# Kernel optimization log

Measured on AMD Instinct MI355X. Metric: run time of the kernel, lower is better.

The kernel has to match this reference:

```python
import jax, jax.numpy as jnp
import numpy as np

T, B, I, H, O = 512, 64, 512, 1024, 512
STDV = 1.0 / np.sqrt(H)


def setup_inputs() -> dict:
    key = jax.random.key(0)
    ks = jax.random.split(key, 12)
    u = lambda k, shape: jax.random.uniform(k, shape, jnp.float32, -STDV, STDV)
    return {
        "input": jax.random.normal(ks[0], (T, B, I), jnp.float32),
        "state": jnp.zeros((B, H), jnp.float32),
        "W_zh": u(ks[1], (H, H)), "W_zx": u(ks[2], (I, H)), "b_z": u(ks[3], (H,)),
        "W_rh": u(ks[4], (H, H)), "W_rx": u(ks[5], (I, H)), "b_r": u(ks[6], (H,)),
        "W_hh": u(ks[7], (H, H)), "W_hx": u(ks[8], (I, H)), "b_h": u(ks[9], (H,)),
        "W_out": u(ks[10], (O, H)), "b_out": u(ks[11], (O,)),
    }


def reference(input, state, W_zh, W_zx, b_z, W_rh, W_rx, b_r, W_hh, W_hx, b_h, W_out, b_out):
    # input: [T, B, I]; state: [B, H]
    def step(h, x):
        z = jax.nn.sigmoid(h @ W_zh + x @ W_zx + b_z)
        r = jax.nn.sigmoid(h @ W_rh + x @ W_rx + b_r)
        ht = jnp.tanh((h * r) @ W_hh + x @ W_hx + b_h)
        h = (1.0 - z) * h + z * ht
        y = h @ W_out.T + b_out  # Linear(hidim -> outdim)
        return h, y

    h_final, Y = jax.lax.scan(step, state, input)  # Y: [T, B, O]
    # torch.cat(Y, dim=0) -> [T*B, O]
    return Y.reshape(T * B, O), h_final
```

## Files before the change

### kernel.cpp

```cpp
#include <hip/hip_runtime.h>
#include <cstdint>


#define TT 512
#define BB 64
#define II 512
#define HH 1024
#define OO 512
#define NTHR 1024
#define NBLK 256
#define RSTR 528

typedef float4 f4;
__device__ __forceinline__ f4 ld4(const float* p){ return *reinterpret_cast<const f4*>(p); }
__device__ __forceinline__ int swz(int k){ return k ^ (((k >> 4) & 7) << 2); }

__device__ __forceinline__ void ldc4(const float* p, f4* d){
  asm volatile(
    "global_load_dwordx4 %0, %4, off sc0 sc1\n\t"
    "global_load_dwordx4 %1, %4, off offset:256 sc0 sc1\n\t"
    "global_load_dwordx4 %2, %4, off offset:512 sc0 sc1\n\t"
    "global_load_dwordx4 %3, %4, off offset:768 sc0 sc1\n\t"
    "s_waitcnt vmcnt(0)"
    : "=&v"(d[0]),"=&v"(d[1]),"=&v"(d[2]),"=&v"(d[3])
    : "v"(p) : "memory");
}
__device__ __forceinline__ float ldc1(const float* p){
  float v;
  asm volatile("global_load_dword %0, %1, off sc0 sc1\n\ts_waitcnt vmcnt(0)"
               : "=v"(v) : "v"(p) : "memory");
  return v;
}
__device__ __forceinline__ void stc1(float* p, float v){
  asm volatile("global_store_dword %0, %1, off sc0 sc1" :: "v"(p), "v"(v) : "memory");
}

__global__ void k_transpose_x(const float* __restrict__ x, float* __restrict__ xT){
  size_t total = (size_t)TT * II * BB;
  for (size_t n = (size_t)blockIdx.x * blockDim.x + threadIdx.x; n < total;
       n += (size_t)gridDim.x * blockDim.x){
    size_t t = n / ((size_t)II * BB);
    size_t rem = n % ((size_t)II * BB);
    size_t i = rem / BB, b = rem % BB;
    xT[n] = x[(t * BB + b) * II + i];
  }
}

__global__ void k_transpose_wx(const float* __restrict__ W, float* __restrict__ WT){
  size_t n = (size_t)blockIdx.x * blockDim.x + threadIdx.x;
  if (n >= (size_t)II * HH) return;
  size_t j = n / II, k = n % II;
  WT[n] = W[k * HH + j];
}

__global__ void k_transpose_h0(const float* __restrict__ st, float* __restrict__ h0){
  size_t n = (size_t)blockIdx.x * blockDim.x + threadIdx.x;
  if (n >= (size_t)HH * BB) return;
  size_t j = n / BB, b = n % BB;
  h0[n] = st[b * HH + j];
}

__global__ void k_init_bars(unsigned* bars){
  if (threadIdx.x < 512) bars[threadIdx.x] = 0;
}

__device__ __forceinline__ void g_arrive(unsigned* bars, int bid, unsigned ep){
  asm volatile("s_waitcnt vmcnt(0)" ::: "memory");
  unsigned* leaf = bars + (bid & 15) * 16;
  unsigned old = __hip_atomic_fetch_add(leaf, 1u, __ATOMIC_RELAXED, __HIP_MEMORY_SCOPE_AGENT);
  if (old + 1u == ep * 16u)
    __hip_atomic_fetch_add(bars + 256, 1u, __ATOMIC_RELAXED, __HIP_MEMORY_SCOPE_AGENT);
}
__device__ __forceinline__ void g_wait(unsigned* bars, unsigned ep){
  while (__hip_atomic_load(bars + 256, __ATOMIC_RELAXED, __HIP_MEMORY_SCOPE_AGENT) < ep * 16u)
    __builtin_amdgcn_s_sleep(1);
}

#define WREDUCE(v) { v += __shfl_xor(v, 16); v += __shfl_xor(v, 32); }

__global__ __launch_bounds__(NTHR) void k_gru(
    const float* __restrict__ xT,
    const float* __restrict__ WxTr, const float* __restrict__ WxTz, const float* __restrict__ WxTh,
    float* __restrict__ h, float* __restrict__ s,
    const float* __restrict__ W_zh, const float* __restrict__ b_z,
    const float* __restrict__ W_rh, const float* __restrict__ b_r,
    const float* __restrict__ W_hh, const float* __restrict__ b_h,
    const float* __restrict__ W_out, const float* __restrict__ b_out,
    float* __restrict__ out, unsigned* __restrict__ bars)
{
  __shared__ float sW[3 * 4 * 1024];
  __shared__ float red[16 * RSTR];
  __shared__ float xpre[3][256];
  __shared__ float sZ[256];
  __shared__ float sBias[16];

  const int tid = threadIdx.x;
  const int bid = blockIdx.x;
  const int j0 = bid * 4, o0 = bid * 2;

  {
    const int k = tid;
    f4 vr = ld4(W_rh + (size_t)k * HH + j0);
    f4 vz = ld4(W_zh + (size_t)k * HH + j0);
    f4 vh = ld4(W_hh + (size_t)k * HH + j0);
    const int kx = swz(k);
    float ar[4] = {vr.x,vr.y,vr.z,vr.w};
    float az[4] = {vz.x,vz.y,vz.z,vz.w};
    float ah[4] = {vh.x,vh.y,vh.z,vh.w};
    #pragma unroll
    for (int c = 0; c < 4; ++c){
      sW[0*4096 + c*1024 + kx] = ar[c];
      sW[1*4096 + c*1024 + kx] = az[c];
      sW[2*4096 + c*1024 + kx] = ah[c];
    }
  }
  if (tid < 4){
    sBias[tid]     = b_r[j0 + tid];
    sBias[4 + tid] = b_z[j0 + tid];
    sBias[8 + tid] = b_h[j0 + tid];
    if (tid < 2) sBias[12 + tid] = b_out[o0 + tid];
  }

  const int bg = tid & 15, b0 = bg * 4;
  const int ksec = tid >> 4;
  const int wv = tid >> 6;
  const bool wr0 = ((tid & 48) == 0);
  const int kh0 = ksec * 16;
  const int kx0 = ksec * 8;
  __syncthreads();

  for (int t = -1; t < TT; ++t){
    if (t >= 0){
      const float* hb = h + kh0 * BB + b0;

      {
        float aR[4][4] = {};
        #pragma unroll
        for (int i4 = 0; i4 < 4; ++i4){
          f4 hv4[4];
          ldc4(hb + i4*4*BB, hv4);
          const int kxc = swz(kh0 + i4*4);
          #pragma unroll
          for (int c = 0; c < 4; ++c){
            f4 wf = *reinterpret_cast<const f4*>(&sW[0*4096 + c*1024 + kxc]);
            float wvv[4] = {wf.x, wf.y, wf.z, wf.w};
            #pragma unroll
            for (int kk = 0; kk < 4; ++kk){
              const f4 hv = hv4[kk];
              aR[c][0] = fmaf(wvv[kk], hv.x, aR[c][0]);
              aR[c][1] = fmaf(wvv[kk], hv.y, aR[c][1]);
              aR[c][2] = fmaf(wvv[kk], hv.z, aR[c][2]);
              aR[c][3] = fmaf(wvv[kk], hv.w, aR[c][3]);
            }
          }
        }
        #pragma unroll
        for (int c = 0; c < 4; ++c)
          #pragma unroll
          for (int bb = 0; bb < 4; ++bb) WREDUCE(aR[c][bb]);
        if (wr0)
          #pragma unroll
          for (int c = 0; c < 4; ++c)
            #pragma unroll
            for (int bb = 0; bb < 4; ++bb)
              red[wv*RSTR + c*64 + b0 + bb] = aR[c][bb];
      }
      __syncthreads();
      if (tid < 256){
        float sum = 0.f;
        #pragma unroll
        for (int w = 0; w < 16; ++w) sum += red[w*RSTR + tid];
        const int c = tid >> 6, bl = tid & 63;
        const float v = sum + xpre[0][tid] + sBias[c];
        const float rr = 1.f / (1.f + expf(-v));
        const int jg = j0 + c;
        stc1(&s[jg*BB + bl], rr * ldc1(&h[jg*BB + bl]));
      }
      __syncthreads();
      if (tid == 0) g_arrive(bars, bid, 2*t + 1);

      {
        float aZ[4][4] = {};
        float aY[2][4] = {};
        #pragma unroll
        for (int i4 = 0; i4 < 4; ++i4){
          f4 hv4[4];
          ldc4(hb + i4*4*BB, hv4);
          const int kc = kh0 + i4*4;
          const int kxc = swz(kc);
          #pragma unroll
          for (int c = 0; c < 4; ++c){
            f4 wf = *reinterpret_cast<const f4*>(&sW[1*4096 + c*1024 + kxc]);
            float wvv[4] = {wf.x, wf.y, wf.z, wf.w};
            #pragma unroll
            for (int kk = 0; kk < 4; ++kk){
              const f4 hv = hv4[kk];
              aZ[c][0] = fmaf(wvv[kk], hv.x, aZ[c][0]);
              aZ[c][1] = fmaf(wvv[kk], hv.y, aZ[c][1]);
              aZ[c][2] = fmaf(wvv[kk], hv.z, aZ[c][2]);
              aZ[c][3] = fmaf(wvv[kk], hv.w, aZ[c][3]);
            }
          }
          #pragma unroll
          for (int oc = 0; oc < 2; ++oc){
            f4 wo = ld4(W_out + (size_t)(o0 + oc) * HH + kc);
            float wvv[4] = {wo.x, wo.y, wo.z, wo.w};
            #pragma unroll
            for (int kk = 0; kk < 4; ++kk){
              const f4 hv = hv4[kk];
              aY[oc][0] = fmaf(wvv[kk], hv.x, aY[oc][0]);
              aY[oc][1] = fmaf(wvv[kk], hv.y, aY[oc][1]);
              aY[oc][2] = fmaf(wvv[kk], hv.z, aY[oc][2]);
              aY[oc][3] = fmaf(wvv[kk], hv.w, aY[oc][3]);
            }
          }
        }
        #pragma unroll
        for (int c = 0; c < 4; ++c)
          #pragma unroll
          for (int bb = 0; bb < 4; ++bb) WREDUCE(aZ[c][bb]);
        #pragma unroll
        for (int oc = 0; oc < 2; ++oc)
          #pragma unroll
          for (int bb = 0; bb < 4; ++bb) WREDUCE(aY[oc][bb]);
        if (wr0){
          #pragma unroll
          for (int c = 0; c < 4; ++c)
            #pragma unroll
            for (int bb = 0; bb < 4; ++bb)
              red[wv*RSTR + c*64 + b0 + bb] = aZ[c][bb];
          #pragma unroll
          for (int oc = 0; oc < 2; ++oc)
            #pragma unroll
            for (int bb = 0; bb < 4; ++bb)
              red[wv*RSTR + 256 + oc*64 + b0 + bb] = aY[oc][bb];
        }
      }
      __syncthreads();
      if (tid < 256){
        float sum = 0.f;
        #pragma unroll
        for (int w = 0; w < 16; ++w) sum += red[w*RSTR + tid];
        const int c = tid >> 6;
        sZ[tid] = 1.f / (1.f + expf(-(sum + xpre[1][tid] + sBias[4 + c])));
      } else if (tid < 384){
        const int idx = tid - 256;
        float sum = 0.f;
        #pragma unroll
        for (int w = 0; w < 16; ++w) sum += red[w*RSTR + tid];
        const int oc = idx >> 6, bl = idx & 63;
        if (t > 0)
          out[((size_t)(t-1)*BB + bl)*OO + o0 + oc] = sum + sBias[12 + oc];
      }
      if (tid == 0) g_wait(bars, 2*t + 1);
      __syncthreads();

      {
        float aH[4][4] = {};
        const float* sb = s + kh0 * BB + b0;
        #pragma unroll
        for (int i4 = 0; i4 < 4; ++i4){
          f4 sv4[4];
          ldc4(sb + i4*4*BB, sv4);
          const int kxc = swz(kh0 + i4*4);
          #pragma unroll
          for (int c = 0; c < 4; ++c){
            f4 wf = *reinterpret_cast<const f4*>(&sW[2*4096 + c*1024 + kxc]);
            float wvv[4] = {wf.x, wf.y, wf.z, wf.w};
            #pragma unroll
            for (int kk = 0; kk < 4; ++kk){
              const f4 sv = sv4[kk];
              aH[c][0] = fmaf(wvv[kk], sv.x, aH[c][0]);
              aH[c][1] = fmaf(wvv[kk], sv.y, aH[c][1]);
              aH[c][2] = fmaf(wvv[kk], sv.z, aH[c][2]);
              aH[c][3] = fmaf(wvv[kk], sv.w, aH[c][3]);
            }
          }
        }
        #pragma unroll
        for (int c = 0; c < 4; ++c)
          #pragma unroll
          for (int bb = 0; bb < 4; ++bb) WREDUCE(aH[c][bb]);
        if (wr0)
          #pragma unroll
          for (int c = 0; c < 4; ++c)
            #pragma unroll
            for (int bb = 0; bb < 4; ++bb)
              red[wv*RSTR + c*64 + b0 + bb] = aH[c][bb];
      }
      __syncthreads();
      if (tid < 256){
        float sum = 0.f;
        #pragma unroll
        for (int w = 0; w < 16; ++w) sum += red[w*RSTR + tid];
        const int c = tid >> 6, bl = tid & 63;
        const int jg = j0 + c;
        const float ht = tanhf(sum + xpre[2][tid] + sBias[8 + c]);
        const float z = sZ[tid];
        const float hold = ldc1(&h[jg*BB + bl]);
        const float hnew = fmaf(z, ht - hold, hold);
        stc1(&h[jg*BB + bl], hnew);
        if (t == TT - 1) out[(size_t)TT*BB*OO + (size_t)bl*HH + jg] = hnew;
      }
      __syncthreads();
      if (tid == 0) g_arrive(bars, bid, 2*t + 2);
    }

    if (t + 1 < TT){
      const int tc = t + 1;
      const float* xb = xT + (size_t)tc * II * BB + kx0 * BB + b0;
      #pragma unroll
      for (int g = 0; g < 3; ++g){
        const float* Wg = (g == 0) ? WxTr : (g == 1) ? WxTz : WxTh;
        {
          float aX[4][4] = {};
          #pragma unroll
          for (int i4 = 0; i4 < 2; ++i4){
            f4 xv4[4];
            #pragma unroll
            for (int kk = 0; kk < 4; ++kk) xv4[kk] = ld4(xb + (i4*4+kk) * BB);
            #pragma unroll
            for (int c = 0; c < 4; ++c){
              f4 wf = ld4(Wg + (size_t)(j0 + c) * II + kx0 + i4*4);
              float wvv[4] = {wf.x, wf.y, wf.z, wf.w};
              #pragma unroll
              for (int kk = 0; kk < 4; ++kk){
                const f4 xv = xv4[kk];
                aX[c][0] = fmaf(wvv[kk], xv.x, aX[c][0]);
                aX[c][1] = fmaf(wvv[kk], xv.y, aX[c][1]);
                aX[c][2] = fmaf(wvv[kk], xv.z, aX[c][2]);
                aX[c][3] = fmaf(wvv[kk], xv.w, aX[c][3]);
              }
            }
          }
          #pragma unroll
          for (int c = 0; c < 4; ++c)
            #pragma unroll
            for (int bb = 0; bb < 4; ++bb) WREDUCE(aX[c][bb]);
          if (wr0)
            #pragma unroll
            for (int c = 0; c < 4; ++c)
              #pragma unroll
              for (int bb = 0; bb < 4; ++bb)
                red[wv*RSTR + c*64 + b0 + bb] = aX[c][bb];
        }
        __syncthreads();
        if (tid < 256){
          float sum = 0.f;
          #pragma unroll
          for (int w = 0; w < 16; ++w) sum += red[w*RSTR + tid];
          xpre[g][tid] = sum;
        }
        __syncthreads();
      }
    }

    if (t >= 0){
      if (tid == 0) g_wait(bars, 2*t + 2);
      __syncthreads();
    }
  }

  {
    float aY[2][4] = {};
    const float* hb = h + kh0 * BB + b0;
    #pragma unroll
    for (int i4 = 0; i4 < 4; ++i4){
      f4 hv4[4];
      ldc4(hb + i4*4*BB, hv4);
      const int kc = kh0 + i4*4;
      #pragma unroll
      for (int oc = 0; oc < 2; ++oc){
        f4 wo = ld4(W_out + (size_t)(o0 + oc) * HH + kc);
        float wvv[4] = {wo.x, wo.y, wo.z, wo.w};
        #pragma unroll
        for (int kk = 0; kk < 4; ++kk){
          const f4 hv = hv4[kk];
          aY[oc][0] = fmaf(wvv[kk], hv.x, aY[oc][0]);
          aY[oc][1] = fmaf(wvv[kk], hv.y, aY[oc][1]);
          aY[oc][2] = fmaf(wvv[kk], hv.z, aY[oc][2]);
          aY[oc][3] = fmaf(wvv[kk], hv.w, aY[oc][3]);
        }
      }
    }
    #pragma unroll
    for (int oc = 0; oc < 2; ++oc)
      #pragma unroll
      for (int bb = 0; bb < 4; ++bb) WREDUCE(aY[oc][bb]);
    if (wr0)
      #pragma unroll
      for (int oc = 0; oc < 2; ++oc)
        #pragma unroll
        for (int bb = 0; bb < 4; ++bb)
          red[wv*RSTR + oc*64 + b0 + bb] = aY[oc][bb];
    __syncthreads();
    if (tid < 128){
      float sum = 0.f;
      #pragma unroll
      for (int w = 0; w < 16; ++w) sum += red[w*RSTR + tid];
      const int oc = tid >> 6, bl = tid & 63;
      out[((size_t)(TT-1)*BB + bl)*OO + o0 + oc] = sum + sBias[12 + oc];
    }
  }
}

extern "C" void kernel_launch(void* const* d_in, const int* in_sizes, int n_in,
                              void* d_out, int out_size, void* d_ws, size_t ws_size,
                              hipStream_t stream) {
  const float* x     = (const float*)d_in[0];
  const float* st    = (const float*)d_in[1];
  const float* W_zh  = (const float*)d_in[2];
  const float* W_zx  = (const float*)d_in[3];
  const float* b_z   = (const float*)d_in[4];
  const float* W_rh  = (const float*)d_in[5];
  const float* W_rx  = (const float*)d_in[6];
  const float* b_r   = (const float*)d_in[7];
  const float* W_hh  = (const float*)d_in[8];
  const float* W_hx  = (const float*)d_in[9];
  const float* b_h   = (const float*)d_in[10];
  const float* W_out = (const float*)d_in[11];
  const float* b_out = (const float*)d_in[12];
  float* out = (float*)d_out;
  float* ws  = (float*)d_ws;

  const size_t xT_sz = (size_t)TT * II * BB;
  const size_t wx_sz = (size_t)II * HH;
  const size_t h_sz  = (size_t)HH * BB;
  const size_t need  = (xT_sz + 3*wx_sz + 2*h_sz) * sizeof(float) + 512*sizeof(unsigned);
  if (ws_size < need) return;

  float* xT   = ws;
  float* WxTr = xT + xT_sz;
  float* WxTz = WxTr + wx_sz;
  float* WxTh = WxTz + wx_sz;
  float* h    = WxTh + wx_sz;
  float* s    = h + h_sz;
  unsigned* bars = (unsigned*)(s + h_sz);

  k_transpose_x <<<8192, 256, 0, stream>>>(x, xT);
  k_transpose_wx<<<2048, 256, 0, stream>>>(W_rx, WxTr);
  k_transpose_wx<<<2048, 256, 0, stream>>>(W_zx, WxTz);
  k_transpose_wx<<<2048, 256, 0, stream>>>(W_hx, WxTh);
  k_transpose_h0<<< 256, 256, 0, stream>>>(st, h);
  k_init_bars   <<<   1, 512, 0, stream>>>(bars);

  k_gru<<<NBLK, NTHR, 0, stream>>>(xT, WxTr, WxTz, WxTh, h, s,
                                   W_zh, b_z, W_rh, b_r, W_hh, b_h,
                                   W_out, b_out, out, bars);
}
```

Baseline: 15.19 ms.

## Fuse r/z/out passes, double-buffer h, and hide x-projection behind grid barriers

Merges the r-gate, z-gate and output-projection matvecs into one pass over h, so h is read once and there is one reduction sync instead of two. Ping-pong buffers for h let the new state be written without overwriting the old one. The x-projection work for the next timestep is split across the gaps between arriving at and waiting on the two grid barriers, so that work overlaps barrier latency. This costs more registers and a larger reduction buffer in LDS, and the h·W_hh loads are widened to eight vectors per batch.

```diff
diff --git a/kernel.cpp b/kernel.cpp
--- a/kernel.cpp
+++ b/kernel.cpp
@@ -9,7 +9,7 @@
 #define OO 512
 #define NTHR 1024
 #define NBLK 256
-#define RSTR 528
+#define RSTR 656
 
 typedef float4 f4;
 __device__ __forceinline__ f4 ld4(const float* p){ return *reinterpret_cast<const f4*>(p); }
@@ -25,6 +25,21 @@
     : "=&v"(d[0]),"=&v"(d[1]),"=&v"(d[2]),"=&v"(d[3])
     : "v"(p) : "memory");
 }
+__device__ __forceinline__ void ldc8(const float* p, f4* d){
+  asm volatile(
+    "global_load_dwordx4 %0, %8, off sc0 sc1\n\t"
+    "global_load_dwordx4 %1, %8, off offset:256 sc0 sc1\n\t"
+    "global_load_dwordx4 %2, %8, off offset:512 sc0 sc1\n\t"
+    "global_load_dwordx4 %3, %8, off offset:768 sc0 sc1\n\t"
+    "global_load_dwordx4 %4, %8, off offset:1024 sc0 sc1\n\t"
+    "global_load_dwordx4 %5, %8, off offset:1280 sc0 sc1\n\t"
+    "global_load_dwordx4 %6, %8, off offset:1536 sc0 sc1\n\t"
+    "global_load_dwordx4 %7, %8, off offset:1792 sc0 sc1\n\t"
+    "s_waitcnt vmcnt(0)"
+    : "=&v"(d[0]),"=&v"(d[1]),"=&v"(d[2]),"=&v"(d[3]),
+      "=&v"(d[4]),"=&v"(d[5]),"=&v"(d[6]),"=&v"(d[7])
+    : "v"(p) : "memory");
+}
 __device__ __forceinline__ float ldc1(const float* p){
   float v;
   asm volatile("global_load_dword %0, %1, off sc0 sc1\n\ts_waitcnt vmcnt(0)"
@@ -81,7 +96,7 @@
 __global__ __launch_bounds__(NTHR) void k_gru(
     const float* __restrict__ xT,
     const float* __restrict__ WxTr, const float* __restrict__ WxTz, const float* __restrict__ WxTh,
-    float* __restrict__ h, float* __restrict__ s,
+    float* __restrict__ h0buf, float* __restrict__ h1buf, float* __restrict__ s,
     const float* __restrict__ W_zh, const float* __restrict__ b_z,
     const float* __restrict__ W_rh, const float* __restrict__ b_r,
     const float* __restrict__ W_hh, const float* __restrict__ b_h,
@@ -129,147 +144,172 @@
   const int kx0 = ksec * 8;
   __syncthreads();
 
+  #define XPRE(g_, tc_) do {                                                 \
+    const float* xb_ = xT + (size_t)(tc_) * II * BB + kx0 * BB + b0;         \
+    const float* Wg_ = ((g_) == 0) ? WxTr : ((g_) == 1) ? WxTz : WxTh;       \
+    float aX_[4][4] = {};                                                    \
+    _Pragma("unroll")                                                        \
+    for (int i4 = 0; i4 < 2; ++i4){                                          \
+      f4 xv4_[4];                                                            \
+      _Pragma("unroll")                                                      \
+      for (int kk = 0; kk < 4; ++kk) xv4_[kk] = ld4(xb_ + (i4*4+kk) * BB);   \
+      _Pragma("unroll")                                                      \
+      for (int c = 0; c < 4; ++c){                                           \
+        f4 wf_ = ld4(Wg_ + (size_t)(j0 + c) * II + kx0 + i4*4);              \
+        float wvv_[4] = {wf_.x, wf_.y, wf_.z, wf_.w};                        \
+        _Pragma("unroll")                                                    \
+        for (int kk = 0; kk < 4; ++kk){                                      \
+          const f4 xv_ = xv4_[kk];                                           \
+          aX_[c][0] = fmaf(wvv_[kk], xv_.x, aX_[c][0]);                      \
+          aX_[c][1] = fmaf(wvv_[kk], xv_.y, aX_[c][1]);                      \
+          aX_[c][2] = fmaf(wvv_[kk], xv_.z, aX_[c][2]);                      \
+          aX_[c][3] = fmaf(wvv_[kk], xv_.w, aX_[c][3]);                      \
+        }                                                                    \
+      }                                                                      \
+    }                                                                        \
+    _Pragma("unroll")                                                        \
+    for (int c = 0; c < 4; ++c)                                              \
+      _Pragma("unroll")                                                      \
+      for (int bb = 0; bb < 4; ++bb) WREDUCE(aX_[c][bb]);                    \
+    if (wr0)                                                                 \
+      _Pragma("unroll")                                                      \
+      for (int c = 0; c < 4; ++c)                                            \
+        _Pragma("unroll")                                                    \
+        for (int bb = 0; bb < 4; ++bb)                                       \
+          red[wv*RSTR + c*64 + b0 + bb] = aX_[c][bb];                        \
+    __syncthreads();                                                         \
+    if (tid < 256){                                                          \
+      float sum_ = 0.f;                                                      \
+      _Pragma("unroll")                                                      \
+      for (int w = 0; w < 16; ++w) sum_ += red[w*RSTR + tid];                \
+      xpre[g_][tid] = sum_;                                                  \
+    }                                                                        \
+    __syncthreads();                                                         \
+  } while (0)
+
   for (int t = -1; t < TT; ++t){
-    if (t >= 0){
-      const float* hb = h + kh0 * BB + b0;
-
-      {
-        float aR[4][4] = {};
-        #pragma unroll
-        for (int i4 = 0; i4 < 4; ++i4){
-          f4 hv4[4];
-          ldc4(hb + i4*4*BB, hv4);
-          const int kxc = swz(kh0 + i4*4);
-          #pragma unroll
-          for (int c = 0; c < 4; ++c){
-            f4 wf = *reinterpret_cast<const f4*>(&sW[0*4096 + c*1024 + kxc]);
-            float wvv[4] = {wf.x, wf.y, wf.z, wf.w};
-            #pragma unroll
-            for (int kk = 0; kk < 4; ++kk){
-              const f4 hv = hv4[kk];
-              aR[c][0] = fmaf(wvv[kk], hv.x, aR[c][0]);
-              aR[c][1] = fmaf(wvv[kk], hv.y, aR[c][1]);
-              aR[c][2] = fmaf(wvv[kk], hv.z, aR[c][2]);
-              aR[c][3] = fmaf(wvv[kk], hv.w, aR[c][3]);
-            }
+    if (t < 0){
+      XPRE(0, 0); XPRE(1, 0); XPRE(2, 0);
+      continue;
+    }
+    const float* hin = (t & 1) ? h1buf : h0buf;
+    float*       hout = (t & 1) ? h0buf : h1buf;
+    const float* hb = hin + kh0 * BB + b0;
+
+    {
+      float aR[4][4] = {}, aZ[4][4] = {}, aY[2][4] = {};
+      #pragma unroll
+      for (int i4 = 0; i4 < 4; ++i4){
+        f4 hv4[4];
+        ldc4(hb + i4*4*BB, hv4);
+        const int kc = kh0 + i4*4;
+        const int kxc = swz(kc);
+        #pragma unroll
+        for (int c = 0; c < 4; ++c){
+          f4 wr_ = *reinterpret_cast<const f4*>(&sW[0*4096 + c*1024 + kxc]);
+          f4 wz_ = *reinterpret_cast<const f4*>(&sW[1*4096 + c*1024 + kxc]);
+          float wrv[4] = {wr_.x, wr_.y, wr_.z, wr_.w};
+          float wzv[4] = {wz_.x, wz_.y, wz_.z, wz_.w};
+          #pragma unroll
+          for (int kk = 0; kk < 4; ++kk){
+            const f4 hv = hv4[kk];
+            aR[c][0] = fmaf(wrv[kk], hv.x, aR[c][0]);
+            aR[c][1] = fmaf(wrv[kk], hv.y, aR[c][1]);
+            aR[c][2] = fmaf(wrv[kk], hv.z, aR[c][2]);
+            aR[c][3] = fmaf(wrv[kk], hv.w, aR[c][3]);
+            aZ[c][0] = fmaf(wzv[kk], hv.x, aZ[c][0]);
+            aZ[c][1] = fmaf(wzv[kk], hv.y, aZ[c][1]);
+            aZ[c][2] = fmaf(wzv[kk], hv.z, aZ[c][2]);
+            aZ[c][3] = fmaf(wzv[kk], hv.w, aZ[c][3]);
           }
         }
         #pragma unroll
-        for (int c = 0; c < 4; ++c)
-          #pragma unroll
-          for (int bb = 0; bb < 4; ++bb) WREDUCE(aR[c][bb]);
-        if (wr0)
-          #pragma unroll
-          for (int c = 0; c < 4; ++c)
-            #pragma unroll
-            for (int bb = 0; bb < 4; ++bb)
-              red[wv*RSTR + c*64 + b0 + bb] = aR[c][bb];
-      }
-      __syncthreads();
-      if (tid < 256){
-        float sum = 0.f;
-        #pragma unroll
-        for (int w = 0; w < 16; ++w) sum += red[w*RSTR + tid];
-        const int c = tid >> 6, bl = tid & 63;
-        const float v = sum + xpre[0][tid] + sBias[c];
-        const float rr = 1.f / (1.f + expf(-v));
-        const int jg = j0 + c;
-        stc1(&s[jg*BB + bl], rr * ldc1(&h[jg*BB + bl]));
-      }
-      __syncthreads();
-      if (tid == 0) g_arrive(bars, bid, 2*t + 1);
-
-      {
-        float aZ[4][4] = {};
-        float aY[2][4] = {};
-        #pragma unroll
-        for (int i4 = 0; i4 < 4; ++i4){
-          f4 hv4[4];
-          ldc4(hb + i4*4*BB, hv4);
-          const int kc = kh0 + i4*4;
-          const int kxc = swz(kc);
-          #pragma unroll
-          for (int c = 0; c < 4; ++c){
-            f4 wf = *reinterpret_cast<const f4*>(&sW[1*4096 + c*1024 + kxc]);
-            float wvv[4] = {wf.x, wf.y, wf.z, wf.w};
-            #pragma unroll
-            for (int kk = 0; kk < 4; ++kk){
-              const f4 hv = hv4[kk];
-              aZ[c][0] = fmaf(wvv[kk], hv.x, aZ[c][0]);
-              aZ[c][1] = fmaf(wvv[kk], hv.y, aZ[c][1]);
-              aZ[c][2] = fmaf(wvv[kk], hv.z, aZ[c][2]);
-              aZ[c][3] = fmaf(wvv[kk], hv.w, aZ[c][3]);
-            }
-          }
-          #pragma unroll
-          for (int oc = 0; oc < 2; ++oc){
-            f4 wo = ld4(W_out + (size_t)(o0 + oc) * HH + kc);
-            float wvv[4] = {wo.x, wo.y, wo.z, wo.w};
-            #pragma unroll
-            for (int kk = 0; kk < 4; ++kk){
-              const f4 hv = hv4[kk];
-              aY[oc][0] = fmaf(wvv[kk], hv.x, aY[oc][0]);
-              aY[oc][1] = fmaf(wvv[kk], hv.y, aY[oc][1]);
-              aY[oc][2] = fmaf(wvv[kk], hv.z, aY[oc][2]);
-              aY[oc][3] = fmaf(wvv[kk], hv.w, aY[oc][3]);
-            }
+        for (int oc = 0; oc < 2; ++oc){
+          f4 wo = ld4(W_out + (size_t)(o0 + oc) * HH + kc);
+          float wvv[4] = {wo.x, wo.y, wo.z, wo.w};
+          #pragma unroll
+          for (int kk = 0; kk < 4; ++kk){
+            const f4 hv = hv4[kk];
+            aY[oc][0] = fmaf(wvv[kk], hv.x, aY[oc][0]);
+            aY[oc][1] = fmaf(wvv[kk], hv.y, aY[oc][1]);
+            aY[oc][2] = fmaf(wvv[kk], hv.z, aY[oc][2]);
+            aY[oc][3] = fmaf(wvv[kk], hv.w, aY[oc][3]);
           }
         }
+      }
+      #pragma unroll
+      for (int c = 0; c < 4; ++c)
+        #pragma unroll
+        for (int bb = 0; bb < 4; ++bb){ WREDUCE(aR[c][bb]); WREDUCE(aZ[c][bb]); }
+      #pragma unroll
+      for (int oc = 0; oc < 2; ++oc)
+        #pragma unroll
+        for (int bb = 0; bb < 4; ++bb) WREDUCE(aY[oc][bb]);
+      if (wr0){
         #pragma unroll
         for (int c = 0; c < 4; ++c)
           #pragma unroll
-          for (int bb = 0; bb < 4; ++bb) WREDUCE(aZ[c][bb]);
+          for (int bb = 0; bb < 4; ++bb){
+            red[wv*RSTR + c*64 + b0 + bb]       = aR[c][bb];
+            red[wv*RSTR + 256 + c*64 + b0 + bb] = aZ[c][bb];
+          }
         #pragma unroll
         for (int oc = 0; oc < 2; ++oc)
           #pragma unroll
-          for (int bb = 0; bb < 4; ++bb) WREDUCE(aY[oc][bb]);
-        if (wr0){
-          #pragma unroll
-          for (int c = 0; c < 4; ++c)
-            #pragma unroll
-            for (int bb = 0; bb < 4; ++bb)
-              red[wv*RSTR + c*64 + b0 + bb] = aZ[c][bb];
-          #pragma unroll
-          for (int oc = 0; oc < 2; ++oc)
-            #pragma unroll
-            for (int bb = 0; bb < 4; ++bb)
-              red[wv*RSTR + 256 + oc*64 + b0 + bb] = aY[oc][bb];
-        }
+          for (int bb = 0; bb < 4; ++bb)
+            red[wv*RSTR + 512 + oc*64 + b0 + bb] = aY[oc][bb];
       }
-      __syncthreads();
-      if (tid < 256){
-        float sum = 0.f;
-        #pragma unroll
-        for (int w = 0; w < 16; ++w) sum += red[w*RSTR + tid];
-        const int c = tid >> 6;
-        sZ[tid] = 1.f / (1.f + expf(-(sum + xpre[1][tid] + sBias[4 + c])));
-      } else if (tid < 384){
-        const int idx = tid - 256;
-        float sum = 0.f;
-        #pragma unroll
-        for (int w = 0; w < 16; ++w) sum += red[w*RSTR + tid];
-        const int oc = idx >> 6, bl = idx & 63;
-        if (t > 0)
-          out[((size_t)(t-1)*BB + bl)*OO + o0 + oc] = sum + sBias[12 + oc];
-      }
-      if (tid == 0) g_wait(bars, 2*t + 1);
-      __syncthreads();
-
-      {
-        float aH[4][4] = {};
-        const float* sb = s + kh0 * BB + b0;
-        #pragma unroll
-        for (int i4 = 0; i4 < 4; ++i4){
-          f4 sv4[4];
-          ldc4(sb + i4*4*BB, sv4);
-          const int kxc = swz(kh0 + i4*4);
+    }
+    __syncthreads();
+    if (tid < 256){
+      float sum = 0.f;
+      #pragma unroll
+      for (int w = 0; w < 16; ++w) sum += red[w*RSTR + tid];
+      const int c = tid >> 6, bl = tid & 63;
+      const float v = sum + xpre[0][tid] + sBias[c];
+      const float rr = 1.f / (1.f + expf(-v));
+      const int jg = j0 + c;
+      stc1(&s[jg*BB + bl], rr * ldc1(&hin[jg*BB + bl]));
+    } else if (tid < 512){
+      const int idx = tid - 256;
+      float sum = 0.f;
+      #pragma unroll
+      for (int w = 0; w < 16; ++w) sum += red[w*RSTR + tid];
+      const int c = idx >> 6;
+      sZ[idx] = 1.f / (1.f + expf(-(sum + xpre[1][idx] + sBias[4 + c])));
+    } else if (tid < 640){
+      const int idx = tid - 512;
+      float sum = 0.f;
+      #pragma unroll
+      for (int w = 0; w < 16; ++w) sum += red[w*RSTR + tid];
+      const int oc = idx >> 6, bl = idx & 63;
+      if (t > 0)
+        out[((size_t)(t-1)*BB + bl)*OO + o0 + oc] = sum + sBias[12 + oc];
+    }
+    __syncthreads();
+    if (tid == 0) g_arrive(bars, bid, 2*t + 1);
+
+    if (t + 1 < TT){ XPRE(0, t+1); XPRE(1, t+1); }
+    if (tid == 0) g_wait(bars, 2*t + 1);
+    __syncthreads();
+
+    {
+      float aH[4][4] = {};
+      const float* sb = s + kh0 * BB + b0;
+      #pragma unroll
+      for (int i8 = 0; i8 < 2; ++i8){
+        f4 sv8[8];
+        ldc8(sb + i8*8*BB, sv8);
+        #pragma unroll
+        for (int q = 0; q < 2; ++q){
+          const int kxc = swz(kh0 + i8*8 + q*4);
           #pragma unroll
           for (int c = 0; c < 4; ++c){
             f4 wf = *reinterpret_cast<const f4*>(&sW[2*4096 + c*1024 + kxc]);
             float wvv[4] = {wf.x, wf.y, wf.z, wf.w};
             #pragma unroll
             for (int kk = 0; kk < 4; ++kk){
-              const f4 sv = sv4[kk];
+              const f4 sv = sv8[q*4+kk];
               aH[c][0] = fmaf(wvv[kk], sv.x, aH[c][0]);
               aH[c][1] = fmaf(wvv[kk], sv.y, aH[c][1]);
               aH[c][2] = fmaf(wvv[kk], sv.z, aH[c][2]);
@@ -277,93 +317,44 @@
             }
           }
         }
+      }
+      #pragma unroll
+      for (int c = 0; c < 4; ++c)
+        #pragma unroll
+        for (int bb = 0; bb < 4; ++bb) WREDUCE(aH[c][bb]);
+      if (wr0)
         #pragma unroll
         for (int c = 0; c < 4; ++c)
           #pragma unroll
-          for (int bb = 0; bb < 4; ++bb) WREDUCE(aH[c][bb]);
-        if (wr0)
-          #pragma unroll
-          for (int c = 0; c < 4; ++c)
-            #pragma unroll
-            for (int bb = 0; bb < 4; ++bb)
-              red[wv*RSTR + c*64 + b0 + bb] = aH[c][bb];
-      }
-      __syncthreads();
-      if (tid < 256){
-        float sum = 0.f;
-        #pragma unroll
-        for (int w = 0; w < 16; ++w) sum += red[w*RSTR + tid];
-        const int c = tid >> 6, bl = tid & 63;
-        const int jg = j0 + c;
-        const float ht = tanhf(sum + xpre[2][tid] + sBias[8 + c]);
-        const float z = sZ[tid];
-        const float hold = ldc1(&h[jg*BB + bl]);
-        const float hnew = fmaf(z, ht - hold, hold);
-        stc1(&h[jg*BB + bl], hnew);
-        if (t == TT - 1) out[(size_t)TT*BB*OO + (size_t)bl*HH + jg] = hnew;
-      }
-      __syncthreads();
-      if (tid == 0) g_arrive(bars, bid, 2*t + 2);
-    }
-
-    if (t + 1 < TT){
-      const int tc = t + 1;
-      const float* xb = xT + (size_t)tc * II * BB + kx0 * BB + b0;
-      #pragma unroll
-      for (int g = 0; g < 3; ++g){
-        const float* Wg = (g == 0) ? WxTr : (g == 1) ? WxTz : WxTh;
-        {
-          float aX[4][4] = {};
-          #pragma unroll
-          for (int i4 = 0; i4 < 2; ++i4){
-            f4 xv4[4];
-            #pragma unroll
-            for (int kk = 0; kk < 4; ++kk) xv4[kk] = ld4(xb + (i4*4+kk) * BB);
-            #pragma unroll
-            for (int c = 0; c < 4; ++c){
-              f4 wf = ld4(Wg + (size_t)(j0 + c) * II + kx0 + i4*4);
-              float wvv[4] = {wf.x, wf.y, wf.z, wf.w};
-              #pragma unroll
-              for (int kk = 0; kk < 4; ++kk){
-                const f4 xv = xv4[kk];
-                aX[c][0] = fmaf(wvv[kk], xv.x, aX[c][0]);
-                aX[c][1] = fmaf(wvv[kk], xv.y, aX[c][1]);
-                aX[c][2] = fmaf(wvv[kk], xv.z, aX[c][2]);
-                aX[c][3] = fmaf(wvv[kk], xv.w, aX[c][3]);
-              }
-            }
-          }
-          #pragma unroll
-          for (int c = 0; c < 4; ++c)
-            #pragma unroll
-            for (int bb = 0; bb < 4; ++bb) WREDUCE(aX[c][bb]);
-          if (wr0)
-            #pragma unroll
-            for (int c = 0; c < 4; ++c)
-              #pragma unroll
-              for (int bb = 0; bb < 4; ++bb)
-                red[wv*RSTR + c*64 + b0 + bb] = aX[c][bb];
-        }
-        __syncthreads();
-        if (tid < 256){
-          float sum = 0.f;
-          #pragma unroll
-          for (int w = 0; w < 16; ++w) sum += red[w*RSTR + tid];
-          xpre[g][tid] = sum;
-        }
-        __syncthreads();
-      }
-    }
-
-    if (t >= 0){
-      if (tid == 0) g_wait(bars, 2*t + 2);
-      __syncthreads();
-    }
+          for (int bb = 0; bb < 4; ++bb)
+            red[wv*RSTR + c*64 + b0 + bb] = aH[c][bb];
+    }
+    __syncthreads();
+    if (tid < 256){
+      float sum = 0.f;
+      #pragma unroll
+      for (int w = 0; w < 16; ++w) sum += red[w*RSTR + tid];
+      const int c = tid >> 6, bl = tid & 63;
+      const int jg = j0 + c;
+      const float ht = tanhf(sum + xpre[2][tid] + sBias[8 + c]);
+      const float z = sZ[tid];
+      const float hold = ldc1(&hin[jg*BB + bl]);
+      const float hnew = fmaf(z, ht - hold, hold);
+      stc1(&hout[jg*BB + bl], hnew);
+      if (t == TT - 1) out[(size_t)TT*BB*OO + (size_t)bl*HH + jg] = hnew;
+    }
+    __syncthreads();
+    if (tid == 0) g_arrive(bars, bid, 2*t + 2);
+
+    if (t + 1 < TT) XPRE(2, t+1);
+    if (tid == 0) g_wait(bars, 2*t + 2);
+    __syncthreads();
   }
 
   {
+    const float* hfin = (TT & 1) ? h1buf : h0buf;
+    const float* hb = hfin + kh0 * BB + b0;
     float aY[2][4] = {};
-    const float* hb = h + kh0 * BB + b0;
     #pragma unroll
     for (int i4 = 0; i4 < 4; ++i4){
       f4 hv4[4];
@@ -402,6 +393,7 @@
       out[((size_t)(TT-1)*BB + bl)*OO + o0 + oc] = sum + sBias[12 + oc];
     }
   }
+  #undef XPRE
 }
 
 extern "C" void kernel_launch(void* const* d_in, const int* in_sizes, int n_in,
@@ -426,25 +418,26 @@
   const size_t xT_sz = (size_t)TT * II * BB;
   const size_t wx_sz = (size_t)II * HH;
   const size_t h_sz  = (size_t)HH * BB;
-  const size_t need  = (xT_sz + 3*wx_sz + 2*h_sz) * sizeof(float) + 512*sizeof(unsigned);
+  const size_t need  = (xT_sz + 3*wx_sz + 3*h_sz) * sizeof(float) + 512*sizeof(unsigned);
   if (ws_size < need) return;
 
   float* xT   = ws;
   float* WxTr = xT + xT_sz;
   float* WxTz = WxTr + wx_sz;
   float* WxTh = WxTz + wx_sz;
-  float* h    = WxTh + wx_sz;
-  float* s    = h + h_sz;
+  float* hb0  = WxTh + wx_sz;
+  float* hb1  = hb0 + h_sz;
+  float* s    = hb1 + h_sz;
   unsigned* bars = (unsigned*)(s + h_sz);
 
   k_transpose_x <<<8192, 256, 0, stream>>>(x, xT);
   k_transpose_wx<<<2048, 256, 0, stream>>>(W_rx, WxTr);
   k_transpose_wx<<<2048, 256, 0, stream>>>(W_zx, WxTz);
   k_transpose_wx<<<2048, 256, 0, stream>>>(W_hx, WxTh);
-  k_transpose_h0<<< 256, 256, 0, stream>>>(st, h);
+  k_transpose_h0<<< 256, 256, 0, stream>>>(st, hb0);
   k_init_bars   <<<   1, 512, 0, stream>>>(bars);
 
-  k_gru<<<NBLK, NTHR, 0, stream>>>(xT, WxTr, WxTz, WxTh, h, s,
+  k_gru<<<NBLK, NTHR, 0, stream>>>(xT, WxTr, WxTz, WxTh, hb0, hb1, s,
                                    W_zh, b_z, W_rh, b_r, W_hh, b_h,
                                    W_out, b_out, out, bars);
 }
```

New measurement: 14.53 ms. 1.05x faster.
